# Kernel tuning notes

Measured on AMD Instinct MI355X. Metric: run time of the kernel, lower is better.

## Reference

```python
import jax, jax.numpy as jnp
import numpy as np

B, N_PER, H, HE = 64, 101, 128, 16
N = B * N_PER
E = B * N_PER * N_PER
L = 3
EPS = 1e-5
NEG_SLOPE = 0.2


def _edge_index():
    nodes = np.arange(N_PER)
    src = np.repeat(nodes, N_PER)  # j (source)
    dst = np.tile(nodes, N_PER)    # i (target)
    offs = np.repeat(np.arange(B) * N_PER, N_PER * N_PER)
    ei = np.stack([np.tile(src, B) + offs, np.tile(dst, B) + offs])
    return jnp.asarray(ei, dtype=jnp.int32)


def setup_inputs() -> dict:
    key = jax.random.key(0)
    ks = jax.random.split(key, 12)
    s = lambda k, shape, sc: (jax.random.normal(k, shape, jnp.float32) * sc)
    inp = {
        "x": jax.random.uniform(ks[0], (N, 2), jnp.float32),
        "demand": jax.random.uniform(ks[1], (N, 1), jnp.float32),
        "edge_attr_in": jax.random.uniform(ks[2], (E, 1), jnp.float32),
        "edge_index": _edge_index(),
        "fc_node_w": s(ks[3], (3, H), 0.3),
        "fc_node_b": jnp.zeros((H,), jnp.float32),
        "bn_g": jnp.ones((H,), jnp.float32),
        "bn_b": jnp.zeros((H,), jnp.float32),
        "fc_edge_w": s(ks[4], (1, HE), 0.3),
        "fc_edge_b": jnp.zeros((HE,), jnp.float32),
        "be_g": jnp.ones((HE,), jnp.float32),
        "be_b": jnp.zeros((HE,), jnp.float32),
        "fc_w": s(ks[5], (L, H, H), 0.08),
        "fc_b": jnp.zeros((L, H), jnp.float32),
        "attn_w": s(ks[6], (L, 2 * H + HE, H), 0.06),
        "attn_b": jnp.zeros((L, H), jnp.float32),
    }
    return inp


def _batchnorm(x, g, b):
    # training-mode BatchNorm1d: batch stats over dim 0, biased variance
    mu = jnp.mean(x, axis=0)
    var = jnp.mean((x - mu) ** 2, axis=0)
    return (x - mu) * jax.lax.rsqrt(var + EPS) * g + b


def _segment_softmax(alpha, seg, num_segments):
    m = jax.ops.segment_max(alpha, seg, num_segments=num_segments)
    a = jnp.exp(alpha - m[seg])
    s = jax.ops.segment_sum(a, seg, num_segments=num_segments)
    return a / (s[seg] + 1e-16)


def reference(x, demand, edge_attr_in, edge_index, fc_node_w, fc_node_b, bn_g, bn_b,
              fc_edge_w, fc_edge_b, be_g, be_b, fc_w, fc_b, attn_w, attn_b):
    src, dst = edge_index[0], edge_index[1]  # j -> i (source_to_target)
    h = jnp.concatenate([x, demand], axis=-1) @ fc_node_w + fc_node_b  # [N,H]
    h = _batchnorm(h, bn_g, bn_b)
    ea = edge_attr_in @ fc_edge_w + fc_edge_b  # [E,HE]
    ea = _batchnorm(ea, be_g, be_b)
    for l in range(L):
        t = h @ fc_w[l] + fc_b[l]                       # [N,H]
        xi, xj = t[dst], t[src]                          # gather per edge
        cat = jnp.concatenate([xi, xj, ea], axis=-1)     # [E, 2H+HE]
        a = cat @ attn_w[l] + attn_b[l]                  # [E,H]
        a = jnp.where(a >= 0, a, NEG_SLOPE * a)          # leaky_relu
        a = _segment_softmax(a, dst, N)                  # per-dest softmax
        out = jax.ops.segment_sum(xj * a, dst, num_segments=N)  # scatter-add
        h = h + out
    return h.reshape(B, N_PER, H)
```

## Files before the change

### kernel.cpp

```cpp
#include <hip/hip_runtime.h>
#include <math.h>

#define NN   6464
#define NPER 101
#define HD   128
#define HE   16
#define NE   652864
#define PERB 10201
#define EPSB 1e-5f
#define SLOPE 0.2f
#define TI   4
#define NBLK 26
#define L2E  1.44269504088896340736f
#define NO   384

typedef __attribute__((ext_vector_type(8))) short bf16x8;
typedef __attribute__((ext_vector_type(4))) float f32x4;

__device__ __forceinline__ unsigned bf16r(float x){
    unsigned u = __float_as_uint(x);
    return (u + 0x7FFFu + ((u >> 16) & 1u)) >> 16;
}
__device__ __forceinline__ unsigned pack2(float lo, float hi){
    return bf16r(lo) | (bf16r(hi) << 16);
}

__global__ __launch_bounds__(256) void k_reduce1(const float* __restrict__ eai, float* __restrict__ part){
    __shared__ float ls[256], ls2[256];
    float s = 0.f, s2 = 0.f;
    for (int i = blockIdx.x*256 + threadIdx.x; i < NE; i += 256*256){
        float v = eai[i]; s += v; s2 += v*v;
    }
    int tid = threadIdx.x;
    ls[tid] = s; ls2[tid] = s2; __syncthreads();
    for (int o = 128; o > 0; o >>= 1){
        if (tid < o){ ls[tid] += ls[tid+o]; ls2[tid] += ls2[tid+o]; }
        __syncthreads();
    }
    if (tid == 0){ part[blockIdx.x] = ls[0]; part[256 + blockIdx.x] = ls2[0]; }
}

__global__ __launch_bounds__(128) void k_comp2(const float* __restrict__ part,
                     const float* __restrict__ few, const float* __restrict__ beg,
                     const float* __restrict__ beb, const float* __restrict__ attn_b,
                     const float* __restrict__ fc_w, const float* __restrict__ fc_b,
                     const float* __restrict__ attn_w,
                     unsigned short* __restrict__ Wt, float* __restrict__ c1, float* __restrict__ dv){
    int blk = blockIdx.x;
    int l = blk / 129, r = blk - l*129;
    int tid = threadIdx.x;
    const float* Wi = attn_w + (size_t)l*272*HD;
    const float* Wj = Wi + HD*HD;
    const float* Fr = (r < HD) ? (fc_w + (size_t)l*HD*HD + (size_t)r*HD) : (fc_b + l*HD);
    float ai = 0.f, aj = 0.f;
    for (int m = 0; m < HD; m++){
        float f = Fr[m];
        ai = fmaf(f, Wi[m*HD + tid], ai);
        aj = fmaf(f, Wj[m*HD + tid], aj);
    }
    if (r < HD){
        unsigned short* Wl = Wt + (size_t)l*NO*HD;
        Wl[(size_t)(      tid)*HD + r] = (unsigned short)bf16r(Fr[tid]);
        Wl[(size_t)(128 + tid)*HD + r] = (unsigned short)bf16r(ai * L2E);
        Wl[(size_t)(256 + tid)*HD + r] = (unsigned short)bf16r(aj * L2E);
    } else {
        __shared__ float red[128], red2[128];
        float s = 0.f, s2 = 0.f;
        for (int t = tid; t < 256; t += 128){ s += part[t]; s2 += part[256 + t]; }
        red[tid] = s; red2[tid] = s2; __syncthreads();
        for (int o = 64; o > 0; o >>= 1){
            if (tid < o){ red[tid] += red[tid+o]; red2[tid] += red2[tid+o]; }
            __syncthreads();
        }
        float mean = red[0] * (1.f/NE);
        float var  = red2[0] * (1.f/NE) - mean*mean;
        __shared__ float sA[HE], sB[HE];
        if (tid < HE){
            float w = few[tid];
            float a = w * rsqrtf(var*w*w + EPSB) * beg[tid];
            sA[tid] = a; sB[tid] = beb[tid] - mean*a;
        }
        __syncthreads();
        const float* W = attn_w + ((size_t)l*272 + 256)*HD;
        float a1 = 0.f, a2 = 0.f;
        for (int k = 0; k < HE; k++){
            float wv = W[k*HD + tid];
            a1 += sA[k]*wv; a2 += sB[k]*wv;
        }
        c1[l*HD + tid] = a1 * L2E;
        dv[l*HD + tid] = (a2 + attn_b[l*HD + tid] + ai + aj) * L2E;
    }
}

__global__ __launch_bounds__(256) void k_node_bn(const float* __restrict__ x, const float* __restrict__ demand,
                          const float* __restrict__ w, const float* __restrict__ b,
                          const float* __restrict__ g, const float* __restrict__ beta,
                          float* __restrict__ hbuf){
    int k = blockIdx.x, tid = threadIdx.x;
    float w0 = w[k], w1 = w[HD+k], w2 = w[2*HD+k], bb = b[k];
    float s = 0.f, s2 = 0.f;
    for (int n = tid; n < NN; n += 256){
        float p = x[2*n]*w0 + x[2*n+1]*w1 + demand[n]*w2 + bb;
        s += p; s2 += p*p;
    }
    __shared__ float ls[256], ls2[256];
    ls[tid] = s; ls2[tid] = s2; __syncthreads();
    for (int o = 128; o > 0; o >>= 1){
        if (tid < o){ ls[tid] += ls[tid+o]; ls2[tid] += ls2[tid+o]; }
        __syncthreads();
    }
    __shared__ float smu, srs;
    if (tid == 0){
        float mu = ls[0]*(1.f/NN);
        float var = ls2[0]*(1.f/NN) - mu*mu;
        smu = mu; srs = rsqrtf(var + EPSB);
    }
    __syncthreads();
    float mu = smu, rs = srs, gg = g[k], be = beta[k];
    for (int n = tid; n < NN; n += 256){
        float p = x[2*n]*w0 + x[2*n+1]*w1 + demand[n]*w2 + bb;
        hbuf[n*HD + k] = (p - mu)*rs*gg + be;
    }
}

__global__ __launch_bounds__(256) void k_prep_es(const float* __restrict__ eai, float* __restrict__ esT){
    int b = blockIdx.x;
    const float* src = eai + (size_t)b*PERB;
    float* dst = esT + (size_t)b*NBLK*NPER*4;
    for (int ji = threadIdx.x; ji < PERB; ji += 256){
        int j = (int)(((unsigned)ji * 10382u) >> 20);
        int i = ji - j*NPER;
        dst[(((size_t)(i >> 2))*NPER + j)*4 + (i & 3)] = src[ji];
    }
}

#define LDA 136
#define LDC 132
__global__ __launch_bounds__(512) void k_gemm16(const float* __restrict__ hbuf,
                     const unsigned short* __restrict__ Wt, const float* __restrict__ fc_b,
                     float* __restrict__ TUV, unsigned* __restrict__ TV16, int l){
    __shared__ short smem[2*128*LDA];
    short* As = smem;
    short* Bt = smem + 128*LDA;
    float* Cs = (float*)smem;

    int bi = blockIdx.x;
    int bm = bi / 3, bn = bi - bm*3;
    int m0 = bm*128, n0g = bn*128;
    int tid = threadIdx.x;

    for (int idx = tid; idx < 128*32; idx += 512){
        int r = idx >> 5, k4 = (idx & 31) * 4;
        int row = m0 + r; if (row > NN-1) row = NN-1;
        float4 v = *(const float4*)&hbuf[(size_t)row*HD + k4];
        ushort4 w4;
        w4.x = (unsigned short)bf16r(v.x); w4.y = (unsigned short)bf16r(v.y);
        w4.z = (unsigned short)bf16r(v.z); w4.w = (unsigned short)bf16r(v.w);
        *(ushort4*)&As[r*LDA + k4] = w4;
    }
    const unsigned short* Wl = Wt + ((size_t)l*NO + n0g)*HD;
    for (int idx = tid; idx < 128*16; idx += 512){
        int n = idx >> 4, c = (idx & 15) * 8;
        *(uint4*)&Bt[n*LDA + c] = *(const uint4*)&Wl[(size_t)n*HD + c];
    }
    __syncthreads();

    int lane = tid & 63, w = tid >> 6;
    int mb = 32*(w & 3), nb = 64*(w >> 2);
    int lm = lane & 15, kg = lane >> 4;
    f32x4 acc[2][4];
    #pragma unroll
    for (int fm = 0; fm < 2; fm++)
        #pragma unroll
        for (int fn = 0; fn < 4; fn++) acc[fm][fn] = (f32x4){0.f,0.f,0.f,0.f};

    #pragma unroll
    for (int kk = 0; kk < 4; kk++){
        int ko = 32*kk + 8*kg;
        bf16x8 a0 = *(bf16x8*)&As[(mb      + lm)*LDA + ko];
        bf16x8 a1 = *(bf16x8*)&As[(mb + 16 + lm)*LDA + ko];
        bf16x8 b0 = *(bf16x8*)&Bt[(nb      + lm)*LDA + ko];
        bf16x8 b1 = *(bf16x8*)&Bt[(nb + 16 + lm)*LDA + ko];
        bf16x8 b2 = *(bf16x8*)&Bt[(nb + 32 + lm)*LDA + ko];
        bf16x8 b3 = *(bf16x8*)&Bt[(nb + 48 + lm)*LDA + ko];
        acc[0][0] = __builtin_amdgcn_mfma_f32_16x16x32_bf16(a0, b0, acc[0][0], 0,0,0);
        acc[0][1] = __builtin_amdgcn_mfma_f32_16x16x32_bf16(a0, b1, acc[0][1], 0,0,0);
        acc[0][2] = __builtin_amdgcn_mfma_f32_16x16x32_bf16(a0, b2, acc[0][2], 0,0,0);
        acc[0][3] = __builtin_amdgcn_mfma_f32_16x16x32_bf16(a0, b3, acc[0][3], 0,0,0);
        acc[1][0] = __builtin_amdgcn_mfma_f32_16x16x32_bf16(a1, b0, acc[1][0], 0,0,0);
        acc[1][1] = __builtin_amdgcn_mfma_f32_16x16x32_bf16(a1, b1, acc[1][1], 0,0,0);
        acc[1][2] = __builtin_amdgcn_mfma_f32_16x16x32_bf16(a1, b2, acc[1][2], 0,0,0);
        acc[1][3] = __builtin_amdgcn_mfma_f32_16x16x32_bf16(a1, b3, acc[1][3], 0,0,0);
    }
    __syncthreads();

    #pragma unroll
    for (int fm = 0; fm < 2; fm++)
        #pragma unroll
        for (int fn = 0; fn < 4; fn++)
            #pragma unroll
            for (int r = 0; r < 4; r++)
                Cs[(mb + 16*fm + 4*kg + r)*LDC + nb + 16*fn + lm] = acc[fm][fn][r];
    __syncthreads();

    if (bn == 1){
        for (int idx = tid; idx < 128*32; idx += 512){
            int r = idx >> 5, c4 = (idx & 31)*4;
            if (m0 + r < NN){
                float4 v = *(float4*)&Cs[r*LDC + c4];
                *(float4*)&TUV[(size_t)(m0+r)*NO + 128 + c4] = v;
            }
        }
    } else {
        int off = (bn == 2) ? 1 : 0;
        const float* fb = fc_b + l*HD;
        for (int idx = tid; idx < 128*64; idx += 512){
            int r = idx >> 6, p = idx & 63;
            if (m0 + r < NN){
                float lo = Cs[r*LDC + 2*p], hi = Cs[r*LDC + 2*p + 1];
                if (bn == 0){ lo += fb[2*p]; hi += fb[2*p+1]; }
                TV16[(size_t)(m0+r)*128 + 2*p + off] = pack2(lo, hi);
            }
        }
    }
}

template<int CNT>
__device__ __forceinline__ void attn_core(const unsigned* tvp, const float4* esp,
                                          float2 c1h, const float2* base,
                                          float2* s, float2* acc){
    constexpr int NCH = (CNT + 3) / 4;
    uint2 A[4], B[4];
    #pragma unroll
    for (int r = 0; r < 4; ++r)
        if (r < CNT) A[r] = *(const uint2*)(tvp + r*128);
    #pragma unroll
    for (int ch = 0; ch < NCH; ++ch){
        const int jb = ch*4;
        #pragma unroll
        for (int r = 0; r < 4; ++r){
            const int jn = jb + 4 + r;
            if (jn < CNT) B[r] = *(const uint2*)(tvp + jn*128);
        }
        #pragma unroll
        for (int r = 0; r < 4; ++r){
            const int j = jb + r;
            if (j < CNT){
                const float4 e4 = esp[j];
                const float ev[4] = {e4.x, e4.y, e4.z, e4.w};
                float tx = __uint_as_float(A[r].x << 16);
                float ty = __uint_as_float(A[r].x & 0xFFFF0000u);
                float vx = __uint_as_float(A[r].y << 16);
                float vy = __uint_as_float(A[r].y & 0xFFFF0000u);
                #pragma unroll
                for (int k = 0; k < TI; ++k){
                    float zx = fmaf(ev[k], c1h.x, base[k].x + vx);
                    float zy = fmaf(ev[k], c1h.y, base[k].y + vy);
                    zx = fmaxf(zx, SLOPE*zx);
                    zy = fmaxf(zy, SLOPE*zy);
                    float wx = __builtin_amdgcn_exp2f(zx);
                    float wy = __builtin_amdgcn_exp2f(zy);
                    s[k].x += wx; s[k].y += wy;
                    acc[k].x = fmaf(wx, tx, acc[k].x);
                    acc[k].y = fmaf(wy, ty, acc[k].y);
                }
            }
        }
        #pragma unroll
        for (int r = 0; r < 4; ++r) A[r] = B[r];
    }
}

__global__ __launch_bounds__(512) void k_attn11(const float* __restrict__ TUV,
                      const unsigned* __restrict__ TV16, const float* __restrict__ esT,
                      const float* __restrict__ c1, const float* __restrict__ dv,
                      float* __restrict__ hbuf, int l, float* __restrict__ outp){
    __shared__ float4 es4[NPER];
    __shared__ float ps[8][TI][HD], pa[8][TI][HD];
    int blk = blockIdx.x;
    int xcd = blk & 7, r = blk >> 3;
    int b = xcd + 8*(r & 7), c = r >> 3;
    int i0 = c*TI;
    int tid = threadIdx.x;
    int q = tid & 63, jg = tid >> 6;
    int h0 = 2*q;

    const float* ep = esT + ((size_t)(b*NBLK + c)*NPER)*4;
    for (int idx = tid; idx < NPER*4; idx += 512)
        ((float*)es4)[idx] = ep[idx];

    float2 c1h = *(const float2*)&c1[l*HD + h0];
    float2 dd  = *(const float2*)&dv[l*HD + h0];
    float2 base[TI], s[TI], acc[TI];
    #pragma unroll
    for (int k = 0; k < TI; k++){
        int i = i0 + k; if (i > NPER-1) i = NPER-1;
        float2 uu = *(const float2*)&TUV[(size_t)(b*NPER + i)*NO + HD + h0];
        base[k].x = uu.x + dd.x; base[k].y = uu.y + dd.y;
        s[k].x = 0.f; s[k].y = 0.f; acc[k].x = 0.f; acc[k].y = 0.f;
    }
    __syncthreads();

    const unsigned* tvp = TV16 + (size_t)(b*NPER + jg*13)*128 + 2*q;
    const float4* esp = es4 + jg*13;
    if (jg < 7) attn_core<13>(tvp, esp, c1h, base, s, acc);
    else        attn_core<10>(tvp, esp, c1h, base, s, acc);

    #pragma unroll
    for (int k = 0; k < TI; k++){
        *(float2*)&ps[jg][k][h0] = s[k];
        *(float2*)&pa[jg][k][h0] = acc[k];
    }
    __syncthreads();
    {
        int k = tid >> 7, h = tid & (HD-1);
        int i = i0 + k;
        if (i < NPER){
            float st = 0.f, at = 0.f;
            #pragma unroll
            for (int g = 0; g < 8; g++){ st += ps[g][k][h]; at += pa[g][k][h]; }
            size_t o = (size_t)(b*NPER + i)*HD + h;
            float res = fmaf(at, __builtin_amdgcn_rcpf(st + 1e-16f), hbuf[o]);
            hbuf[o] = res;
            if (outp) outp[o] = res;
        }
    }
}

extern "C" void kernel_launch(void* const* d_in, const int* in_sizes, int n_in,
                              void* d_out, int out_size, void* d_ws, size_t ws_size,
                              hipStream_t stream) {
    const float* x      = (const float*)d_in[0];
    const float* demand = (const float*)d_in[1];
    const float* eai    = (const float*)d_in[2];
    const float* fnw = (const float*)d_in[4];
    const float* fnb = (const float*)d_in[5];
    const float* bng = (const float*)d_in[6];
    const float* bnb = (const float*)d_in[7];
    const float* few = (const float*)d_in[8];
    const float* beg = (const float*)d_in[10];
    const float* beb = (const float*)d_in[11];
    const float* fcw = (const float*)d_in[12];
    const float* fcb = (const float*)d_in[13];
    const float* aw  = (const float*)d_in[14];
    const float* ab  = (const float*)d_in[15];
    float* out = (float*)d_out;

    float* w     = (float*)d_ws;
    float* hbuf  = w;
    float* TUV   = w + (size_t)NN*HD;
    unsigned* TV16 = (unsigned*)(TUV + (size_t)NN*NO);
    float* esT   = (float*)(TV16 + (size_t)NN*128);
    float* part  = esT + (size_t)64*NBLK*NPER*4;
    float* c1    = part + 512;
    float* dv    = c1 + 3*HD;
    unsigned short* Wt = (unsigned short*)(dv + 3*HD);

    hipLaunchKernelGGL(k_reduce1, dim3(256), dim3(256), 0, stream, eai, part);
    hipLaunchKernelGGL(k_comp2, dim3(3*129), dim3(HD), 0, stream,
                       part, few, beg, beb, ab, fcw, fcb, aw, Wt, c1, dv);
    hipLaunchKernelGGL(k_node_bn, dim3(HD), dim3(256), 0, stream, x, demand, fnw, fnb, bng, bnb, hbuf);
    hipLaunchKernelGGL(k_prep_es, dim3(64), dim3(256), 0, stream, eai, esT);
    for (int l = 0; l < 3; l++){
        hipLaunchKernelGGL(k_gemm16, dim3(51*3), dim3(512), 0, stream,
                           hbuf, Wt, fcb, TUV, TV16, l);
        hipLaunchKernelGGL(k_attn11, dim3(64*NBLK), dim3(512), 0, stream,
                           TUV, TV16, esT, c1, dv, hbuf, l, (l == 2) ? out : (float*)nullptr);
    }
}
```

Measured before the change: 150.7 us.

## Restructure attention: each wave owns two targets over all sources, drop LDS reduction

The attention kernel is reorganized so each block covers 16 target nodes and each wave handles two targets across all 101 sources, instead of 8 waves splitting sources for 4 targets and then combining partial sums through shared memory. This removes the cross-wave LDS reduction and the second barrier, and the edge-attribute layout is changed to 16-wide tiles to match. In exchange the grid shrinks from 1664 to 448 blocks, and each wave runs a long serial loop with less instruction-level parallelism per thread. The source rows are also re-read by 8 waves per block rather than split among them.

```diff
diff --git a/kernel.cpp b/kernel.cpp
--- a/kernel.cpp
+++ b/kernel.cpp
@@ -9,10 +9,9 @@
 #define PERB 10201
 #define EPSB 1e-5f
 #define SLOPE 0.2f
-#define TI   4
-#define NBLK 26
 #define L2E  1.44269504088896340736f
 #define NO   384
+#define NCB  7
 
 typedef __attribute__((ext_vector_type(8))) short bf16x8;
 typedef __attribute__((ext_vector_type(4))) float f32x4;
@@ -126,11 +125,11 @@
 __global__ __launch_bounds__(256) void k_prep_es(const float* __restrict__ eai, float* __restrict__ esT){
     int b = blockIdx.x;
     const float* src = eai + (size_t)b*PERB;
-    float* dst = esT + (size_t)b*NBLK*NPER*4;
+    float* dst = esT + (size_t)b*NCB*NPER*16;
     for (int ji = threadIdx.x; ji < PERB; ji += 256){
         int j = (int)(((unsigned)ji * 10382u) >> 20);
         int i = ji - j*NPER;
-        dst[(((size_t)(i >> 2))*NPER + j)*4 + (i & 3)] = src[ji];
+        dst[(((size_t)(i >> 4))*NPER + j)*16 + (i & 15)] = src[ji];
     }
 }
 
@@ -225,105 +224,98 @@
     }
 }
 
-template<int CNT>
-__device__ __forceinline__ void attn_core(const unsigned* tvp, const float4* esp,
-                                          float2 c1h, const float2* base,
-                                          float2* s, float2* acc){
-    constexpr int NCH = (CNT + 3) / 4;
-    uint2 A[4], B[4];
-    #pragma unroll
-    for (int r = 0; r < 4; ++r)
-        if (r < CNT) A[r] = *(const uint2*)(tvp + r*128);
-    #pragma unroll
-    for (int ch = 0; ch < NCH; ++ch){
-        const int jb = ch*4;
-        #pragma unroll
-        for (int r = 0; r < 4; ++r){
-            const int jn = jb + 4 + r;
-            if (jn < CNT) B[r] = *(const uint2*)(tvp + jn*128);
-        }
-        #pragma unroll
-        for (int r = 0; r < 4; ++r){
-            const int j = jb + r;
-            if (j < CNT){
-                const float4 e4 = esp[j];
-                const float ev[4] = {e4.x, e4.y, e4.z, e4.w};
-                float tx = __uint_as_float(A[r].x << 16);
-                float ty = __uint_as_float(A[r].x & 0xFFFF0000u);
-                float vx = __uint_as_float(A[r].y << 16);
-                float vy = __uint_as_float(A[r].y & 0xFFFF0000u);
-                #pragma unroll
-                for (int k = 0; k < TI; ++k){
-                    float zx = fmaf(ev[k], c1h.x, base[k].x + vx);
-                    float zy = fmaf(ev[k], c1h.y, base[k].y + vy);
-                    zx = fmaxf(zx, SLOPE*zx);
-                    zy = fmaxf(zy, SLOPE*zy);
-                    float wx = __builtin_amdgcn_exp2f(zx);
-                    float wy = __builtin_amdgcn_exp2f(zy);
-                    s[k].x += wx; s[k].y += wy;
-                    acc[k].x = fmaf(wx, tx, acc[k].x);
-                    acc[k].y = fmaf(wy, ty, acc[k].y);
-                }
-            }
-        }
-        #pragma unroll
-        for (int r = 0; r < 4; ++r) A[r] = B[r];
-    }
-}
-
-__global__ __launch_bounds__(512) void k_attn11(const float* __restrict__ TUV,
+__global__ __launch_bounds__(512) void k_attn12(const float* __restrict__ TUV,
                       const unsigned* __restrict__ TV16, const float* __restrict__ esT,
                       const float* __restrict__ c1, const float* __restrict__ dv,
                       float* __restrict__ hbuf, int l, float* __restrict__ outp){
-    __shared__ float4 es4[NPER];
-    __shared__ float ps[8][TI][HD], pa[8][TI][HD];
+    __shared__ float es_s[NPER][16];
     int blk = blockIdx.x;
-    int xcd = blk & 7, r = blk >> 3;
-    int b = xcd + 8*(r & 7), c = r >> 3;
-    int i0 = c*TI;
+    int b = blk & 63, cb = blk >> 6;
+    int i0 = cb*16;
     int tid = threadIdx.x;
-    int q = tid & 63, jg = tid >> 6;
+    int q = tid & 63, w = tid >> 6;
     int h0 = 2*q;
 
-    const float* ep = esT + ((size_t)(b*NBLK + c)*NPER)*4;
-    for (int idx = tid; idx < NPER*4; idx += 512)
-        ((float*)es4)[idx] = ep[idx];
-
+    const float* ep = esT + ((size_t)(b*NCB + cb)*NPER)*16;
+    for (int idx = tid; idx < NPER*16; idx += 512)
+        ((float*)es_s)[idx] = ep[idx];
+
+    int ia = i0 + 2*w, ib = i0 + 2*w + 1;
+    int ca = (ia > NPER-1) ? NPER-1 : ia;
+    int cc = (ib > NPER-1) ? NPER-1 : ib;
     float2 c1h = *(const float2*)&c1[l*HD + h0];
     float2 dd  = *(const float2*)&dv[l*HD + h0];
-    float2 base[TI], s[TI], acc[TI];
-    #pragma unroll
-    for (int k = 0; k < TI; k++){
-        int i = i0 + k; if (i > NPER-1) i = NPER-1;
-        float2 uu = *(const float2*)&TUV[(size_t)(b*NPER + i)*NO + HD + h0];
-        base[k].x = uu.x + dd.x; base[k].y = uu.y + dd.y;
-        s[k].x = 0.f; s[k].y = 0.f; acc[k].x = 0.f; acc[k].y = 0.f;
-    }
-    __syncthreads();
-
-    const unsigned* tvp = TV16 + (size_t)(b*NPER + jg*13)*128 + 2*q;
-    const float4* esp = es4 + jg*13;
-    if (jg < 7) attn_core<13>(tvp, esp, c1h, base, s, acc);
-    else        attn_core<10>(tvp, esp, c1h, base, s, acc);
-
-    #pragma unroll
-    for (int k = 0; k < TI; k++){
-        *(float2*)&ps[jg][k][h0] = s[k];
-        *(float2*)&pa[jg][k][h0] = acc[k];
-    }
-    __syncthreads();
+    float2 uA  = *(const float2*)&TUV[(size_t)(b*NPER + ca)*NO + HD + h0];
+    float2 uB  = *(const float2*)&TUV[(size_t)(b*NPER + cc)*NO + HD + h0];
+    float bax = uA.x + dd.x, bay = uA.y + dd.y;
+    float bbx = uB.x + dd.x, bby = uB.y + dd.y;
+    float sax = 0.f, say = 0.f, aax = 0.f, aay = 0.f;
+    float sbx = 0.f, sby = 0.f, abx = 0.f, aby = 0.f;
+    __syncthreads();
+
+    const unsigned* tvp = TV16 + (size_t)(b*NPER)*128 + h0;
+    const float2* esw = (const float2*)&es_s[0][0] + w;
+    uint2 A = *(const uint2*)tvp;
+    float2 e = *esw;
+    #pragma unroll 4
+    for (int j = 0; j < NPER-1; j++){
+        uint2 An = *(const uint2*)(tvp + 128);
+        float2 en = esw[8];
+        float tx = __uint_as_float(A.x << 16);
+        float ty = __uint_as_float(A.x & 0xFFFF0000u);
+        float vx = __uint_as_float(A.y << 16);
+        float vy = __uint_as_float(A.y & 0xFFFF0000u);
+        float zax = fmaf(e.x, c1h.x, bax + vx);
+        float zay = fmaf(e.x, c1h.y, bay + vy);
+        float zbx = fmaf(e.y, c1h.x, bbx + vx);
+        float zby = fmaf(e.y, c1h.y, bby + vy);
+        zax = fmaxf(zax, SLOPE*zax); zay = fmaxf(zay, SLOPE*zay);
+        zbx = fmaxf(zbx, SLOPE*zbx); zby = fmaxf(zby, SLOPE*zby);
+        float wax = __builtin_amdgcn_exp2f(zax);
+        float way = __builtin_amdgcn_exp2f(zay);
+        float wbx = __builtin_amdgcn_exp2f(zbx);
+        float wby = __builtin_amdgcn_exp2f(zby);
+        sax += wax; say += way; sbx += wbx; sby += wby;
+        aax = fmaf(wax, tx, aax); aay = fmaf(way, ty, aay);
+        abx = fmaf(wbx, tx, abx); aby = fmaf(wby, ty, aby);
+        tvp += 128; esw += 8;
+        A = An; e = en;
+    }
     {
-        int k = tid >> 7, h = tid & (HD-1);
-        int i = i0 + k;
-        if (i < NPER){
-            float st = 0.f, at = 0.f;
-            #pragma unroll
-            for (int g = 0; g < 8; g++){ st += ps[g][k][h]; at += pa[g][k][h]; }
-            size_t o = (size_t)(b*NPER + i)*HD + h;
-            float res = fmaf(at, __builtin_amdgcn_rcpf(st + 1e-16f), hbuf[o]);
-            hbuf[o] = res;
-            if (outp) outp[o] = res;
-        }
+        float tx = __uint_as_float(A.x << 16);
+        float ty = __uint_as_float(A.x & 0xFFFF0000u);
+        float vx = __uint_as_float(A.y << 16);
+        float vy = __uint_as_float(A.y & 0xFFFF0000u);
+        float zax = fmaf(e.x, c1h.x, bax + vx);
+        float zay = fmaf(e.x, c1h.y, bay + vy);
+        float zbx = fmaf(e.y, c1h.x, bbx + vx);
+        float zby = fmaf(e.y, c1h.y, bby + vy);
+        zax = fmaxf(zax, SLOPE*zax); zay = fmaxf(zay, SLOPE*zay);
+        zbx = fmaxf(zbx, SLOPE*zbx); zby = fmaxf(zby, SLOPE*zby);
+        float wax = __builtin_amdgcn_exp2f(zax);
+        float way = __builtin_amdgcn_exp2f(zay);
+        float wbx = __builtin_amdgcn_exp2f(zbx);
+        float wby = __builtin_amdgcn_exp2f(zby);
+        sax += wax; say += way; sbx += wbx; sby += wby;
+        aax = fmaf(wax, tx, aax); aay = fmaf(way, ty, aay);
+        abx = fmaf(wbx, tx, abx); aby = fmaf(wby, ty, aby);
+    }
+
+    if (ia < NPER){
+        size_t o = (size_t)(b*NPER + ia)*HD + h0;
+        float2 hres = *(const float2*)&hbuf[o];
+        hres.x = fmaf(aax, __builtin_amdgcn_rcpf(sax + 1e-16f), hres.x);
+        hres.y = fmaf(aay, __builtin_amdgcn_rcpf(say + 1e-16f), hres.y);
+        *(float2*)&hbuf[o] = hres;
+        if (outp) *(float2*)&outp[o] = hres;
+    }
+    if (ib < NPER){
+        size_t o = (size_t)(b*NPER + ib)*HD + h0;
+        float2 hres = *(const float2*)&hbuf[o];
+        hres.x = fmaf(abx, __builtin_amdgcn_rcpf(sbx + 1e-16f), hres.x);
+        hres.y = fmaf(aby, __builtin_amdgcn_rcpf(sby + 1e-16f), hres.y);
+        *(float2*)&hbuf[o] = hres;
+        if (outp) *(float2*)&outp[o] = hres;
     }
 }
 
@@ -351,7 +343,7 @@
     float* TUV   = w + (size_t)NN*HD;
     unsigned* TV16 = (unsigned*)(TUV + (size_t)NN*NO);
     float* esT   = (float*)(TV16 + (size_t)NN*128);
-    float* part  = esT + (size_t)64*NBLK*NPER*4;
+    float* part  = esT + (size_t)64*NCB*NPER*16;
     float* c1    = part + 512;
     float* dv    = c1 + 3*HD;
     unsigned short* Wt = (unsigned short*)(dv + 3*HD);
@@ -364,7 +356,7 @@
     for (int l = 0; l < 3; l++){
         hipLaunchKernelGGL(k_gemm16, dim3(51*3), dim3(512), 0, stream,
                            hbuf, Wt, fcb, TUV, TV16, l);
-        hipLaunchKernelGGL(k_attn11, dim3(64*NBLK), dim3(512), 0, stream,
+        hipLaunchKernelGGL(k_attn12, dim3(64*NCB), dim3(512), 0, stream,
                            TUV, TV16, esT, c1, dv, hbuf, l, (l == 2) ? out : (float*)nullptr);
     }
 }
```

Result: slower. 161.0 us (+6.8%).

## Fuse edge-stat reduction into edge transpose kernel and vectorize attention math

Applied to the files above, without the earlier changes.

Merges the edge-attribute sum/sum-of-squares reduction into the kernel that transposes edge attributes, so the edge input is read once and one launch is removed. The reduction now produces 64 per-graph partials instead of 256. The attention inner loop is rewritten with two-wide float vector types, so the compiler can emit packed FP32 math. The fused kernel runs with only 64 blocks, which gives less parallelism for the reduction, and the packed-math benefit depends on what the compiler emits.

```diff
diff --git a/kernel.cpp b/kernel.cpp
--- a/kernel.cpp
+++ b/kernel.cpp
@@ -16,6 +16,7 @@
 
 typedef __attribute__((ext_vector_type(8))) short bf16x8;
 typedef __attribute__((ext_vector_type(4))) float f32x4;
+typedef __attribute__((ext_vector_type(2))) float f32x2;
 
 __device__ __forceinline__ unsigned bf16r(float x){
     unsigned u = __float_as_uint(x);
@@ -25,11 +26,19 @@
     return bf16r(lo) | (bf16r(hi) << 16);
 }
 
-__global__ __launch_bounds__(256) void k_reduce1(const float* __restrict__ eai, float* __restrict__ part){
+__global__ __launch_bounds__(256) void k_prep_es(const float* __restrict__ eai, float* __restrict__ esT,
+                         float* __restrict__ part){
     __shared__ float ls[256], ls2[256];
+    int b = blockIdx.x;
+    const float* src = eai + (size_t)b*PERB;
+    float* dst = esT + (size_t)b*NBLK*NPER*4;
     float s = 0.f, s2 = 0.f;
-    for (int i = blockIdx.x*256 + threadIdx.x; i < NE; i += 256*256){
-        float v = eai[i]; s += v; s2 += v*v;
+    for (int ji = threadIdx.x; ji < PERB; ji += 256){
+        int j = (int)(((unsigned)ji * 10382u) >> 20);
+        int i = ji - j*NPER;
+        float v = src[ji];
+        s += v; s2 += v*v;
+        dst[(((size_t)(i >> 2))*NPER + j)*4 + (i & 3)] = v;
     }
     int tid = threadIdx.x;
     ls[tid] = s; ls2[tid] = s2; __syncthreads();
@@ -37,7 +46,7 @@
         if (tid < o){ ls[tid] += ls[tid+o]; ls2[tid] += ls2[tid+o]; }
         __syncthreads();
     }
-    if (tid == 0){ part[blockIdx.x] = ls[0]; part[256 + blockIdx.x] = ls2[0]; }
+    if (tid == 0){ part[b] = ls[0]; part[64 + b] = ls2[0]; }
 }
 
 __global__ __launch_bounds__(128) void k_comp2(const float* __restrict__ part,
@@ -65,8 +74,8 @@
         Wl[(size_t)(256 + tid)*HD + r] = (unsigned short)bf16r(aj * L2E);
     } else {
         __shared__ float red[128], red2[128];
-        float s = 0.f, s2 = 0.f;
-        for (int t = tid; t < 256; t += 128){ s += part[t]; s2 += part[256 + t]; }
+        float s = (tid < 64) ? part[tid] : 0.f;
+        float s2 = (tid < 64) ? part[64 + tid] : 0.f;
         red[tid] = s; red2[tid] = s2; __syncthreads();
         for (int o = 64; o > 0; o >>= 1){
             if (tid < o){ red[tid] += red[tid+o]; red2[tid] += red2[tid+o]; }
@@ -120,17 +129,6 @@
     for (int n = tid; n < NN; n += 256){
         float p = x[2*n]*w0 + x[2*n+1]*w1 + demand[n]*w2 + bb;
         hbuf[n*HD + k] = (p - mu)*rs*gg + be;
-    }
-}
-
-__global__ __launch_bounds__(256) void k_prep_es(const float* __restrict__ eai, float* __restrict__ esT){
-    int b = blockIdx.x;
-    const float* src = eai + (size_t)b*PERB;
-    float* dst = esT + (size_t)b*NBLK*NPER*4;
-    for (int ji = threadIdx.x; ji < PERB; ji += 256){
-        int j = (int)(((unsigned)ji * 10382u) >> 20);
-        int i = ji - j*NPER;
-        dst[(((size_t)(i >> 2))*NPER + j)*4 + (i & 3)] = src[ji];
     }
 }
 
@@ -227,8 +225,8 @@
 
 template<int CNT>
 __device__ __forceinline__ void attn_core(const unsigned* tvp, const float4* esp,
-                                          float2 c1h, const float2* base,
-                                          float2* s, float2* acc){
+                                          f32x2 c1h, const f32x2* base,
+                                          f32x2* s, f32x2* acc){
     constexpr int NCH = (CNT + 3) / 4;
     uint2 A[4], B[4];
     #pragma unroll
@@ -248,21 +246,20 @@
             if (j < CNT){
                 const float4 e4 = esp[j];
                 const float ev[4] = {e4.x, e4.y, e4.z, e4.w};
-                float tx = __uint_as_float(A[r].x << 16);
-                float ty = __uint_as_float(A[r].x & 0xFFFF0000u);
-                float vx = __uint_as_float(A[r].y << 16);
-                float vy = __uint_as_float(A[r].y & 0xFFFF0000u);
+                f32x2 t2, v2;
+                t2.x = __uint_as_float(A[r].x << 16);
+                t2.y = __uint_as_float(A[r].x & 0xFFFF0000u);
+                v2.x = __uint_as_float(A[r].y << 16);
+                v2.y = __uint_as_float(A[r].y & 0xFFFF0000u);
                 #pragma unroll
                 for (int k = 0; k < TI; ++k){
-                    float zx = fmaf(ev[k], c1h.x, base[k].x + vx);
-                    float zy = fmaf(ev[k], c1h.y, base[k].y + vy);
-                    zx = fmaxf(zx, SLOPE*zx);
-                    zy = fmaxf(zy, SLOPE*zy);
-                    float wx = __builtin_amdgcn_exp2f(zx);
-                    float wy = __builtin_amdgcn_exp2f(zy);
-                    s[k].x += wx; s[k].y += wy;
-                    acc[k].x = fmaf(wx, tx, acc[k].x);
-                    acc[k].y = fmaf(wy, ty, acc[k].y);
+                    f32x2 z = ev[k]*c1h + (base[k] + v2);
+                    z = __builtin_elementwise_max(z, z*SLOPE);
+                    f32x2 wv;
+                    wv.x = __builtin_amdgcn_exp2f(z.x);
+                    wv.y = __builtin_amdgcn_exp2f(z.y);
+                    s[k] += wv;
+                    acc[k] += wv * t2;
                 }
             }
         }
@@ -289,15 +286,15 @@
     for (int idx = tid; idx < NPER*4; idx += 512)
         ((float*)es4)[idx] = ep[idx];
 
-    float2 c1h = *(const float2*)&c1[l*HD + h0];
-    float2 dd  = *(const float2*)&dv[l*HD + h0];
-    float2 base[TI], s[TI], acc[TI];
+    f32x2 c1h = *(const f32x2*)&c1[l*HD + h0];
+    f32x2 dd  = *(const f32x2*)&dv[l*HD + h0];
+    f32x2 base[TI], s[TI], acc[TI];
     #pragma unroll
     for (int k = 0; k < TI; k++){
         int i = i0 + k; if (i > NPER-1) i = NPER-1;
-        float2 uu = *(const float2*)&TUV[(size_t)(b*NPER + i)*NO + HD + h0];
-        base[k].x = uu.x + dd.x; base[k].y = uu.y + dd.y;
-        s[k].x = 0.f; s[k].y = 0.f; acc[k].x = 0.f; acc[k].y = 0.f;
+        f32x2 uu = *(const f32x2*)&TUV[(size_t)(b*NPER + i)*NO + HD + h0];
+        base[k] = uu + dd;
+        s[k] = (f32x2){0.f, 0.f}; acc[k] = (f32x2){0.f, 0.f};
     }
     __syncthreads();
 
@@ -308,8 +305,8 @@
 
     #pragma unroll
     for (int k = 0; k < TI; k++){
-        *(float2*)&ps[jg][k][h0] = s[k];
-        *(float2*)&pa[jg][k][h0] = acc[k];
+        *(f32x2*)&ps[jg][k][h0] = s[k];
+        *(f32x2*)&pa[jg][k][h0] = acc[k];
     }
     __syncthreads();
     {
@@ -352,15 +349,14 @@
     unsigned* TV16 = (unsigned*)(TUV + (size_t)NN*NO);
     float* esT   = (float*)(TV16 + (size_t)NN*128);
     float* part  = esT + (size_t)64*NBLK*NPER*4;
-    float* c1    = part + 512;
+    float* c1    = part + 128;
     float* dv    = c1 + 3*HD;
     unsigned short* Wt = (unsigned short*)(dv + 3*HD);
 
-    hipLaunchKernelGGL(k_reduce1, dim3(256), dim3(256), 0, stream, eai, part);
+    hipLaunchKernelGGL(k_prep_es, dim3(64), dim3(256), 0, stream, eai, esT, part);
     hipLaunchKernelGGL(k_comp2, dim3(3*129), dim3(HD), 0, stream,
                        part, few, beg, beb, ab, fcw, fcb, aw, Wt, c1, dv);
     hipLaunchKernelGGL(k_node_bn, dim3(HD), dim3(256), 0, stream, x, demand, fnw, fnb, bng, bnb, hbuf);
-    hipLaunchKernelGGL(k_prep_es, dim3(64), dim3(256), 0, stream, eai, esT);
     for (int l = 0; l < 3; l++){
         hipLaunchKernelGGL(k_gemm16, dim3(51*3), dim3(512), 0, stream,
                            hbuf, Wt, fcb, TUV, TV16, l);
```

New measurement: 150.9 us. Within noise of the previous version (+0.1%).
